# Optimization experiments

Hardware: AMD Instinct MI355X
Metric: run time of the kernel (lower is better)

Reference implementation:

```python
import jax, jax.numpy as jnp
import numpy as np

B, L, D_IN, HID, D_OUT = 1024, 100, 32, 128, 32
STEP = 0.05


def setup_inputs() -> dict:
    key = jax.random.key(0)
    ks = jax.random.split(key, 16)
    s = lambda fan_in: 1.0 / np.sqrt(fan_in)
    coeffs = jax.random.normal(ks[0], (B, L, D_IN), dtype=jnp.float32)
    times = (jnp.arange(L, dtype=jnp.float32) * STEP)
    # initial: Linear(input_dim -> hidden_dim)
    init_w = jax.random.uniform(ks[1], (HID, D_IN), minval=-s(D_IN), maxval=s(D_IN))
    init_b = jax.random.uniform(ks[2], (HID,), minval=-s(D_IN), maxval=s(D_IN))
    # vector field MLP: hidden -> hidden -> hidden -> hidden*input_dim (tanh)
    fw0 = jax.random.uniform(ks[3], (HID, HID), minval=-s(HID), maxval=s(HID))
    fb0 = jax.random.uniform(ks[4], (HID,), minval=-s(HID), maxval=s(HID))
    fw1 = jax.random.uniform(ks[5], (HID, HID), minval=-s(HID), maxval=s(HID))
    fb1 = jax.random.uniform(ks[6], (HID,), minval=-s(HID), maxval=s(HID))
    fw2 = jax.random.uniform(ks[7], (HID, HID), minval=-s(HID), maxval=s(HID))
    fb2 = jax.random.uniform(ks[8], (HID,), minval=-s(HID), maxval=s(HID))
    fwf = jax.random.uniform(ks[9], (HID * D_IN, HID), minval=-s(HID), maxval=s(HID))
    fbf = jax.random.uniform(ks[10], (HID * D_IN,), minval=-s(HID), maxval=s(HID))
    # decoder: Linear(hidden -> output_dim)
    dec_w = jax.random.uniform(ks[11], (D_OUT, HID), minval=-s(HID), maxval=s(HID))
    dec_b = jax.random.uniform(ks[12], (D_OUT,), minval=-s(HID), maxval=s(HID))
    return {"coeffs": coeffs, "times": times, "init_w": init_w, "init_b": init_b,
            "fw0": fw0, "fb0": fb0, "fw1": fw1, "fb1": fb1, "fw2": fw2, "fb2": fb2,
            "fwf": fwf, "fbf": fbf, "dec_w": dec_w, "dec_b": dec_b}


def reference(coeffs, times, init_w, init_b, fw0, fb0, fw1, fb1, fw2, fb2, fwf, fbf, dec_w, dec_b):
    b = coeffs.shape[0]

    def vf(z, dxdt):
        # CDE vector field: MLP(z) -> [B, HID, D_IN] matrix, contracted with dX/dt
        h = jnp.tanh(z @ fw0.T + fb0)
        h = jnp.tanh(h @ fw1.T + fb1)
        h = jnp.tanh(h @ fw2.T + fb2)
        h = jnp.tanh(h @ fwf.T + fbf)              # [B, HID*D_IN]
        f = h.reshape(b, HID, D_IN)
        return jnp.einsum('bhd,bd->bh', f, dxdt)   # dz/dt, [B, HID]

    # y0 = initial(X.evaluate(times))[:, 0, :]; linear interpolation on the
    # knot grid evaluates to the coefficients themselves at knot times.
    z0 = coeffs[:, 0, :] @ init_w.T + init_b       # [B, HID]

    dts = times[1:] - times[:-1]                                   # [L-1]
    slopes = (coeffs[:, 1:, :] - coeffs[:, :-1, :]) / dts[None, :, None]
    slopes = jnp.transpose(slopes, (1, 0, 2))                      # [L-1, B, D_IN]

    def rk4_step(z, xs):
        dt, dxdt = xs
        k1 = vf(z, dxdt)
        k2 = vf(z + 0.5 * dt * k1, dxdt)
        k3 = vf(z + 0.5 * dt * k2, dxdt)
        k4 = vf(z + dt * k3, dxdt)
        z_new = z + (dt / 6.0) * (k1 + 2.0 * k2 + 2.0 * k3 + k4)
        return z_new, z_new

    _, zs = jax.lax.scan(rk4_step, z0, (dts, slopes))              # [L-1, B, HID]
    z = jnp.concatenate([z0[None], zs], axis=0)                    # [L, B, HID]
    z = jnp.transpose(z, (1, 0, 2))                                # [B, L, HID]
    return z @ dec_w.T + dec_b                                     # [B, L, D_OUT]
```

## Files before the change

### kernel.cpp

```cpp
#include <hip/hip_runtime.h>

#define B_TOT 1024
#define L_T   100
#define DIN   32
#define HID   128
#define DOUT  32
#define BT    32
#define NHG   8
#define NBLK  256
#define NTHREADS 1024

typedef _Float16 half8 __attribute__((ext_vector_type(8)));
typedef float    f32x4 __attribute__((ext_vector_type(4)));

#define SWZ(r,c) (((r) << 7) + ((c) ^ (((r) & 7) << 3)))

__device__ __forceinline__ float fast_exp2(float x){
#if __has_builtin(__builtin_amdgcn_exp2f)
  return __builtin_amdgcn_exp2f(x);
#else
  float r; asm("v_exp_f32 %0, %1\n\ts_nop 1" : "=v"(r) : "v"(x)); return r;
#endif
}
__device__ __forceinline__ float fast_rcp(float x){
#if __has_builtin(__builtin_amdgcn_rcpf)
  return __builtin_amdgcn_rcpf(x);
#else
  float r; asm("v_rcp_f32 %0, %1\n\ts_nop 1" : "=v"(r) : "v"(x)); return r;
#endif
}
__device__ __forceinline__ float fast_tanh(float x){
  float e = fast_exp2(x * 2.885390081777926f);
  return 1.0f - 2.0f * fast_rcp(e + 1.0f);
}

__global__ void reorder_w(const float* __restrict__ src, _Float16* __restrict__ dst,
                          int N, int K){
  int id = blockIdx.x * 256 + threadIdx.x;
  if (id >= N * K) return;
  int n = id / K, k = id - n * K;
  int tile = n >> 4, nl = n & 15;
  int kq = (k >> 3) & 3, k0 = k >> 5, ki = k & 7;
  int lane = nl + (kq << 4);
  int K32 = K >> 5;
  dst[(((tile * K32 + k0) << 6) + lane) * 8 + ki] = (_Float16)src[id];
}

__global__ __launch_bounds__(NTHREADS) void cde_main(
    const float* __restrict__ coeffs, const float* __restrict__ times,
    const float* __restrict__ init_b, const float* __restrict__ fb0,
    const float* __restrict__ fb1,    const float* __restrict__ fb2,
    const float* __restrict__ fbf,    const float* __restrict__ dec_b,
    const _Float16* __restrict__ W,   float* __restrict__ dzg,
    unsigned int* __restrict__ flags, float* __restrict__ out)
{
  __shared__ _Float16 wslice[32*2048];
  __shared__ _Float16 bufA[BT*HID];
  __shared__ _Float16 bufB[BT*HID];
  __shared__ float    dzs[BT][16];
  __shared__ float    dxs[BT][DIN];
  __shared__ float    fbfs[512];

  const int tid  = threadIdx.x;
  const int lane = tid & 63;
  const int w    = tid >> 6;
  const int cl   = lane & 15;
  const int g    = lane >> 4;
  const int hg   = blockIdx.x & 7;
  const int bt   = blockIdx.x >> 3;
  const int b0   = bt * BT;
  const int cr   = tid >> 5;
  const int cc   = (tid & 31) * 4;

  const _Float16* W0 = W;
  const _Float16* W1 = W + 16384;
  const _Float16* W2 = W + 32768;
  const _Float16* Wf = W + 49152;
  const _Float16* Wi = W + 573440;
  const _Float16* Wd = W + 577536;
  const _Float16* Wfs = Wf + hg * 32 * 2048;
  unsigned int* flag = flags + bt * 32;

  auto bar = [&]{
    __builtin_amdgcn_sched_barrier(0);
    asm volatile("s_waitcnt lgkmcnt(0)" ::: "memory");
    __builtin_amdgcn_s_barrier();
    __builtin_amdgcn_sched_barrier(0);
    asm volatile("" ::: "memory");
  };

  if (tid < 512) fbfs[tid] = fbf[hg*512 + tid];

  float* scratch = (float*)wslice;
  {
    int r = tid >> 5, d = tid & 31;
    bufB[SWZ(r, d)] = (_Float16)coeffs[(b0 + r)*(L_T*DIN) + d];
  }
  bar();
  {
    const int rt = w >> 3, ct = w & 7;
    f32x4 acc = {0.f,0.f,0.f,0.f};
    half8 a = *(const half8*)(bufB + SWZ(rt*16 + cl, 8*g));
    half8 b = *(const half8*)(Wi + (ct*64 + lane)*8);
    acc = __builtin_amdgcn_mfma_f32_16x16x32_f16(a, b, acc, 0, 0, 0);
    float bn = init_b[ct*16 + cl];
#pragma unroll
    for (int r = 0; r < 4; ++r){
      float v = acc[r] + bn;
      scratch[(rt*16 + 4*g + r)*128 + ct*16 + cl] = v;
      bufA[SWZ(rt*16 + 4*g + r, ct*16 + cl)] = (_Float16)v;
    }
  }
  bar();
  float zf[4], ka[4] = {0.f,0.f,0.f,0.f};
#pragma unroll
  for (int j = 0; j < 4; ++j) zf[j] = scratch[cr*128 + cc + j];
  bar();
  for (int i = tid*8; i < 32*2048; i += NTHREADS*8)
    *(half8*)(wslice + i) = *(const half8*)(Wfs + i);
  bar();

#define DENSE(IN, OB, WT, BIAS) {                                          \
    const int rt = w >> 3, ct = w & 7;                                     \
    f32x4 acc = {0.f,0.f,0.f,0.f};                                         \
    _Pragma("unroll")                                                      \
    for (int kq = 0; kq < 4; ++kq){                                        \
      half8 a = *(const half8*)((IN) + SWZ(rt*16 + cl, kq*32 + 8*g));      \
      half8 b = *(const half8*)((WT) + ((ct*4 + kq)*64 + lane)*8);         \
      acc = __builtin_amdgcn_mfma_f32_16x16x32_f16(a, b, acc, 0,0,0);}     \
    float bn = (BIAS)[ct*16 + cl];                                         \
    _Pragma("unroll")                                                      \
    for (int r = 0; r < 4; ++r)                                            \
      (OB)[SWZ(rt*16 + 4*g + r, ct*16 + cl)] = (_Float16)fast_tanh(acc[r] + bn); }

#define DECODER(TS) {                                                      \
    const int rt = w >> 1, ct = w & 1;                                     \
    f32x4 acc = {0.f,0.f,0.f,0.f};                                         \
    _Pragma("unroll")                                                      \
    for (int kq = 0; kq < 4; ++kq){                                        \
      half8 a = *(const half8*)(bufA + SWZ(rt*16 + cl, kq*32 + 8*g));      \
      half8 b = *(const half8*)(Wd + ((ct*4 + kq)*64 + lane)*8);           \
      acc = __builtin_amdgcn_mfma_f32_16x16x32_f16(a, b, acc, 0,0,0);}     \
    float bn = dec_b[ct*16 + cl];                                          \
    _Pragma("unroll")                                                      \
    for (int r = 0; r < 4; ++r)                                            \
      out[(b0 + rt*16 + 4*g + r)*(L_T*DOUT) + (TS)*DOUT + ct*16 + cl] = acc[r] + bn; }

  const int rt_b = w & 1, hp = w >> 1;
  float dxlo[4], dxhi[4];

  for (int t = 0; t < L_T - 1; ++t){
    if (hg == 0 && w < 4) DECODER(t)

    float dt = times[t+1] - times[t];
    {
      int r = tid >> 5, d = tid & 31;
      const float* cp = coeffs + (b0 + r)*(L_T*DIN) + t*DIN + d;
      dxs[r][d] = (cp[DIN] - cp[0]) / dt;
    }
    bar();
#pragma unroll
    for (int r = 0; r < 4; ++r){
      dxlo[r] = dxs[rt_b*16 + 4*g + r][cl];
      dxhi[r] = dxs[rt_b*16 + 4*g + r][16 + cl];
    }

    for (int s = 0; s < 4; ++s){
      DENSE(bufA, bufB, W0, fb0)
      bar();
      DENSE(bufB, bufA, W1, fb1)
      bar();
      DENSE(bufA, bufB, W2, fb2)
      bar();

      {
        half8 af[4];
#pragma unroll
        for (int kq = 0; kq < 4; ++kq)
          af[kq] = *(const half8*)(bufB + SWZ(rt_b*16 + cl, kq*32 + 8*g));
#pragma unroll
        for (int hl2 = 0; hl2 < 2; ++hl2){
          const int hl = 2*hp + hl2;
          const _Float16* tpA = wslice + (2*hl)*2048 + lane*8;
          const _Float16* tpB = tpA + 2048;
          f32x4 aA = {0.f,0.f,0.f,0.f}, aB = {0.f,0.f,0.f,0.f};
#pragma unroll
          for (int j = 0; j < 4; ++j)
            aA = __builtin_amdgcn_mfma_f32_16x16x32_f16(af[j], *(const half8*)(tpA + 512*j), aA, 0,0,0);
#pragma unroll
          for (int j = 0; j < 4; ++j)
            aB = __builtin_amdgcn_mfma_f32_16x16x32_f16(af[j], *(const half8*)(tpB + 512*j), aB, 0,0,0);
          float bnA = fbfs[(2*hl)*16 + cl], bnB = fbfs[(2*hl + 1)*16 + cl];
          float p[4];
#pragma unroll
          for (int r = 0; r < 4; ++r)
            p[r] = fast_tanh(aA[r] + bnA)*dxlo[r] + fast_tanh(aB[r] + bnB)*dxhi[r];
#pragma unroll
          for (int m = 1; m < 16; m <<= 1){
#pragma unroll
            for (int r = 0; r < 4; ++r) p[r] += __shfl_xor(p[r], m, 64);
          }
          if (cl == 0){
#pragma unroll
            for (int r = 0; r < 4; ++r) dzs[rt_b*16 + 4*g + r][hl] = p[r];
          }
        }
      }
      bar();

      float* dbuf = dzg + ((4*t + s) & 1) * (B_TOT*HID);
      if (tid < 512){
        int br = tid >> 4, hl = tid & 15;
        __hip_atomic_store(&dbuf[(b0 + br)*HID + hg*16 + hl], dzs[br][hl],
                           __ATOMIC_RELAXED, __HIP_MEMORY_SCOPE_AGENT);
      }
      asm volatile("s_waitcnt vmcnt(0)" ::: "memory");
      bar();
      const unsigned int epoch = (unsigned int)(4*t + s + 1);
      if (tid == 0){
        __hip_atomic_fetch_add(flag, 1u, __ATOMIC_RELAXED, __HIP_MEMORY_SCOPE_AGENT);
        while (__hip_atomic_load(flag, __ATOMIC_RELAXED, __HIP_MEMORY_SCOPE_AGENT)
               < 8u * epoch)
          __builtin_amdgcn_s_sleep(2);
      }
      bar();
      float kv[4];
      {
        const float* src = dbuf + (b0 + cr)*HID + cc;
#pragma unroll
        for (int j = 0; j < 4; ++j)
          kv[j] = __hip_atomic_load(&src[j], __ATOMIC_RELAXED,
                                    __HIP_MEMORY_SCOPE_AGENT);
      }
#pragma unroll
      for (int j = 0; j < 4; ++j){
        float nin;
        if (s == 0){ ka[j] = kv[j];        nin = zf[j] + 0.5f*dt*kv[j]; }
        else if (s == 1){ ka[j] += 2.f*kv[j]; nin = zf[j] + 0.5f*dt*kv[j]; }
        else if (s == 2){ ka[j] += 2.f*kv[j]; nin = zf[j] + dt*kv[j]; }
        else { zf[j] += (dt*(1.f/6.f))*(ka[j] + kv[j]); nin = zf[j]; }
        bufA[SWZ(cr, cc + j)] = (_Float16)nin;
      }
      bar();
    }
  }
  if (hg == 0 && w < 4) DECODER(L_T - 1)
}

extern "C" void kernel_launch(void* const* d_in, const int* in_sizes, int n_in,
                              void* d_out, int out_size, void* d_ws, size_t ws_size,
                              hipStream_t stream){
  const float* coeffs = (const float*)d_in[0];
  const float* times  = (const float*)d_in[1];
  const float* init_w = (const float*)d_in[2];
  const float* init_b = (const float*)d_in[3];
  const float* fw0    = (const float*)d_in[4];
  const float* fb0    = (const float*)d_in[5];
  const float* fw1    = (const float*)d_in[6];
  const float* fb1    = (const float*)d_in[7];
  const float* fw2    = (const float*)d_in[8];
  const float* fb2    = (const float*)d_in[9];
  const float* fwf    = (const float*)d_in[10];
  const float* fbf    = (const float*)d_in[11];
  const float* dec_w  = (const float*)d_in[12];
  const float* dec_b  = (const float*)d_in[13];
  _Float16* W  = (_Float16*)d_ws;
  float* dzg   = (float*)((char*)d_ws + 1163264);
  unsigned int* flags = (unsigned int*)((char*)d_ws + 2211840);
  float* outf  = (float*)d_out;

  hipLaunchKernelGGL(reorder_w, dim3(64),   dim3(256), 0, stream, fw0, W,          128, 128);
  hipLaunchKernelGGL(reorder_w, dim3(64),   dim3(256), 0, stream, fw1, W + 16384,  128, 128);
  hipLaunchKernelGGL(reorder_w, dim3(64),   dim3(256), 0, stream, fw2, W + 32768,  128, 128);
  hipLaunchKernelGGL(reorder_w, dim3(2048), dim3(256), 0, stream, fwf, W + 49152,  4096, 128);
  hipLaunchKernelGGL(reorder_w, dim3(16),   dim3(256), 0, stream, init_w, W + 573440, 128, 32);
  hipLaunchKernelGGL(reorder_w, dim3(16),   dim3(256), 0, stream, dec_w,  W + 577536,  32, 128);
  hipMemsetAsync(flags, 0, 32 * 128, stream);

  void* kargs[] = {(void*)&coeffs, (void*)&times, (void*)&init_b, (void*)&fb0,
                   (void*)&fb1, (void*)&fb2, (void*)&fbf, (void*)&dec_b,
                   (void*)&W, (void*)&dzg, (void*)&flags, (void*)&outf};
  hipLaunchCooperativeKernel((const void*)cde_main, dim3(NBLK), dim3(NTHREADS),
                             kargs, 0, stream);
}
```

Before: 3.264 ms.

## Pack exchanged dz to fp16, per-wave flag arrivals, prefetch coeffs, rotate decoder

```diff
diff --git a/kernel.cpp b/kernel.cpp
--- a/kernel.cpp
+++ b/kernel.cpp
@@ -51,7 +51,7 @@
     const float* __restrict__ init_b, const float* __restrict__ fb0,
     const float* __restrict__ fb1,    const float* __restrict__ fb2,
     const float* __restrict__ fbf,    const float* __restrict__ dec_b,
-    const _Float16* __restrict__ W,   float* __restrict__ dzg,
+    const _Float16* __restrict__ W,   unsigned int* __restrict__ dzg,
     unsigned int* __restrict__ flags, float* __restrict__ out)
 {
   __shared__ _Float16 wslice[32*2048];
@@ -149,14 +149,20 @@
   const int rt_b = w & 1, hp = w >> 1;
   float dxlo[4], dxhi[4];
 
+  float pc0, pc1;
+  {
+    int r = tid >> 5, d = tid & 31;
+    const float* cp = coeffs + (b0 + r)*(L_T*DIN) + d;
+    pc0 = cp[0]; pc1 = cp[DIN];
+  }
+
   for (int t = 0; t < L_T - 1; ++t){
-    if (hg == 0 && w < 4) DECODER(t)
+    if (hg == (t & 7) && w < 4) DECODER(t)
 
     float dt = times[t+1] - times[t];
     {
       int r = tid >> 5, d = tid & 31;
-      const float* cp = coeffs + (b0 + r)*(L_T*DIN) + t*DIN + d;
-      dxs[r][d] = (cp[DIN] - cp[0]) / dt;
+      dxs[r][d] = (pc1 - pc0) / dt;
     }
     bar();
 #pragma unroll
@@ -166,6 +172,11 @@
     }
 
     for (int s = 0; s < 4; ++s){
+      if (s == 3 && t < L_T - 2){
+        int r = tid >> 5, d = tid & 31;
+        const float* cp = coeffs + (b0 + r)*(L_T*DIN) + (t+1)*DIN + d;
+        pc0 = cp[0]; pc1 = cp[DIN];
+      }
       DENSE(bufA, bufB, W0, fb0)
       bar();
       DENSE(bufB, bufA, W1, fb1)
@@ -208,29 +219,37 @@
       }
       bar();
 
-      float* dbuf = dzg + ((4*t + s) & 1) * (B_TOT*HID);
-      if (tid < 512){
-        int br = tid >> 4, hl = tid & 15;
-        __hip_atomic_store(&dbuf[(b0 + br)*HID + hg*16 + hl], dzs[br][hl],
+      unsigned int* dbuf = dzg + ((4*t + s) & 1) * (B_TOT * 64);
+      if (tid < 256){
+        int br = tid >> 3, hlp = tid & 7;
+        unsigned int lo = (unsigned int)__builtin_bit_cast(
+                              unsigned short, (_Float16)dzs[br][2*hlp]);
+        unsigned int hi = (unsigned int)__builtin_bit_cast(
+                              unsigned short, (_Float16)dzs[br][2*hlp + 1]);
+        __hip_atomic_store(&dbuf[(b0 + br)*64 + hg*8 + hlp], lo | (hi << 16),
                            __ATOMIC_RELAXED, __HIP_MEMORY_SCOPE_AGENT);
       }
       asm volatile("s_waitcnt vmcnt(0)" ::: "memory");
-      bar();
       const unsigned int epoch = (unsigned int)(4*t + s + 1);
+      if (w < 8 && lane == 0)
+        __hip_atomic_fetch_add(flag, 1u, __ATOMIC_RELAXED, __HIP_MEMORY_SCOPE_AGENT);
       if (tid == 0){
-        __hip_atomic_fetch_add(flag, 1u, __ATOMIC_RELAXED, __HIP_MEMORY_SCOPE_AGENT);
         while (__hip_atomic_load(flag, __ATOMIC_RELAXED, __HIP_MEMORY_SCOPE_AGENT)
-               < 8u * epoch)
+               < 64u * epoch)
           __builtin_amdgcn_s_sleep(2);
       }
       bar();
       float kv[4];
       {
-        const float* src = dbuf + (b0 + cr)*HID + cc;
-#pragma unroll
-        for (int j = 0; j < 4; ++j)
-          kv[j] = __hip_atomic_load(&src[j], __ATOMIC_RELAXED,
-                                    __HIP_MEMORY_SCOPE_AGENT);
+        const unsigned int* src = dbuf + (b0 + cr)*64 + (tid & 31)*2;
+        unsigned int p0 = __hip_atomic_load(&src[0], __ATOMIC_RELAXED,
+                                            __HIP_MEMORY_SCOPE_AGENT);
+        unsigned int p1 = __hip_atomic_load(&src[1], __ATOMIC_RELAXED,
+                                            __HIP_MEMORY_SCOPE_AGENT);
+        kv[0] = (float)__builtin_bit_cast(_Float16, (unsigned short)(p0 & 0xffff));
+        kv[1] = (float)__builtin_bit_cast(_Float16, (unsigned short)(p0 >> 16));
+        kv[2] = (float)__builtin_bit_cast(_Float16, (unsigned short)(p1 & 0xffff));
+        kv[3] = (float)__builtin_bit_cast(_Float16, (unsigned short)(p1 >> 16));
       }
 #pragma unroll
       for (int j = 0; j < 4; ++j){
@@ -244,7 +263,7 @@
       bar();
     }
   }
-  if (hg == 0 && w < 4) DECODER(L_T - 1)
+  if (hg == ((L_T - 1) & 7) && w < 4) DECODER(L_T - 1)
 }
 
 extern "C" void kernel_launch(void* const* d_in, const int* in_sizes, int n_in,
@@ -265,7 +284,7 @@
   const float* dec_w  = (const float*)d_in[12];
   const float* dec_b  = (const float*)d_in[13];
   _Float16* W  = (_Float16*)d_ws;
-  float* dzg   = (float*)((char*)d_ws + 1163264);
+  unsigned int* dzg   = (unsigned int*)((char*)d_ws + 1163264);
   unsigned int* flags = (unsigned int*)((char*)d_ws + 2211840);
   float* outf  = (float*)d_out;
 
```

After: 3.706 ms. 13.6% more time.
